# Performance work log

Measured on AMD Instinct MI355X. Metric: run time of the kernel, lower is better.

The kernel has to match this reference:

```python
import jax, jax.numpy as jnp
import numpy as np

NUM_USER = 20000
NUM_ITEM = 20000
N = NUM_USER + NUM_ITEM
E = 250000
DIM_X = 64
NEG_SLOPE = 0.01  # F.leaky_relu default
EPS = 1e-12


def _xavier(key, shape):
    scale = (2.0 / (shape[0] + shape[1])) ** 0.5
    return jax.random.normal(key, shape, dtype=jnp.float32) * scale


def setup_inputs() -> dict:
    key = jax.random.key(0)
    ks = iter(jax.random.split(key, 64))
    inp = {}
    feat_dims = {'v': 2048, 'a': 128, 't': 100}
    lat_dims = {'v': 256, 'a': 128, 't': 100}
    for m in ('v', 'a', 't'):
        Fd, L = feat_dims[m], lat_dims[m]
        inp[m + '_feat'] = jax.random.normal(next(ks), (NUM_ITEM, Fd), dtype=jnp.float32)
        inp[m + '_pref'] = _xavier(next(ks), (NUM_USER, L))
        inp[m + '_mlp_w'] = _xavier(next(ks), (Fd, L))
        inp[m + '_mlp_b'] = jnp.zeros((L,), jnp.float32)
        inp[m + '_conv_w'] = _xavier(next(ks), (L, L))
        inp[m + '_conv_b'] = jnp.zeros((L,), jnp.float32)
        inp[m + '_lin_w'] = _xavier(next(ks), (L, DIM_X))
        inp[m + '_lin_b'] = jnp.zeros((DIM_X,), jnp.float32)
        inp[m + '_g_w'] = _xavier(next(ks), (L, DIM_X))
        inp[m + '_g_b'] = jnp.zeros((DIM_X,), jnp.float32)
    inp['id_emb'] = _xavier(next(ks), (N, DIM_X))
    src = jax.random.randint(next(ks), (E,), 0, NUM_USER)
    dst = jax.random.randint(next(ks), (E,), NUM_USER, N)
    inp['edge_index'] = jnp.stack([src, dst])  # [2, E] user->item
    inp['user_nodes'] = jax.random.randint(next(ks), (1024,), 0, NUM_USER)
    inp['pos_items'] = jax.random.randint(next(ks), (1024,), NUM_USER, N)
    inp['neg_items'] = jax.random.randint(next(ks), (1024,), NUM_USER, N)
    return inp


def _l2norm(x):
    return x / jnp.maximum(jnp.linalg.norm(x, axis=-1, keepdims=True), EPS)


def _graph_gat(x, src, dst, w, b):
    # x: [N, L] -> per-edge gather, gated attention, scatter-add (aggr='add')
    xw = x @ w                      # [N, L]
    x_j = xw[src]                   # source (neighbor) features, [E, L]
    x_i = xw[dst]                   # destination features, [E, L]
    inner = jnp.sum(x_i * x_j, axis=-1)                      # [E]
    deg = jax.ops.segment_sum(jnp.ones_like(inner), src, num_segments=N)
    gate = jax.nn.sigmoid(inner * (deg[src] ** -0.5))        # degree-scaled gate
    logits = inner * gate
    seg_max = jax.ops.segment_max(logits, dst, num_segments=N)
    e = jnp.exp(logits - seg_max[dst])
    denom = jax.ops.segment_sum(e, dst, num_segments=N)
    alpha = e / jnp.maximum(denom[dst], 1e-16)               # softmax over in-edges of dst
    out = jax.ops.segment_sum(x_j * alpha[:, None], dst, num_segments=N)
    return _l2norm(out + b)


def _gnn(feat, pref, mlp_w, mlp_b, conv_w, conv_b, lin_w, lin_b, g_w, g_b, id_emb, src, dst):
    temp = jnp.tanh(feat @ mlp_w + mlp_b)                    # [num_item, L]
    x = _l2norm(jnp.concatenate([pref, temp], axis=0))        # [N, L]
    h = jax.nn.leaky_relu(_graph_gat(x, src, dst, conv_w, conv_b), NEG_SLOPE)
    x_hat = jax.nn.leaky_relu(x @ lin_w + lin_b, NEG_SLOPE) + id_emb
    return jax.nn.leaky_relu(h @ g_w + g_b + x_hat, NEG_SLOPE)  # [N, 64]


def reference(v_feat, a_feat, t_feat,
              v_pref, v_mlp_w, v_mlp_b, v_conv_w, v_conv_b, v_lin_w, v_lin_b, v_g_w, v_g_b,
              a_pref, a_mlp_w, a_mlp_b, a_conv_w, a_conv_b, a_lin_w, a_lin_b, a_g_w, a_g_b,
              t_pref, t_mlp_w, t_mlp_b, t_conv_w, t_conv_b, t_lin_w, t_lin_b, t_g_w, t_g_b,
              id_emb, edge_index, user_nodes, pos_items, neg_items):
    # __init__ doubles the edge list with its reverse (undirected graph)
    ei = jnp.concatenate([edge_index, edge_index[::-1]], axis=1)
    src, dst = ei[0], ei[1]
    v_rep = _gnn(v_feat, v_pref, v_mlp_w, v_mlp_b, v_conv_w, v_conv_b, v_lin_w, v_lin_b, v_g_w, v_g_b, id_emb, src, dst)
    a_rep = _gnn(a_feat, a_pref, a_mlp_w, a_mlp_b, a_conv_w, a_conv_b, a_lin_w, a_lin_b, a_g_w, a_g_b, id_emb, src, dst)
    t_rep = _gnn(t_feat, t_pref, t_mlp_w, t_mlp_b, t_conv_w, t_conv_b, t_lin_w, t_lin_b, t_g_w, t_g_b, id_emb, src, dst)
    rep = (v_rep + a_rep + t_rep) / 3.0                      # [N, 64]
    pos_scores = jnp.sum(rep[user_nodes] * rep[pos_items], axis=1)
    neg_scores = jnp.sum(rep[user_nodes] * rep[neg_items], axis=1)
    return (pos_scores, neg_scores)
```

## Files before the change

kernel.cpp:

```cpp
#include <hip/hip_runtime.h>
#include <math.h>

#define NUSER 20000
#define NITEM 20000
#define NNODE 40000
#define MP_USER 20096
#define MP_NODE 40064

typedef unsigned short u16;
typedef __attribute__((ext_vector_type(8))) short bf16x8;
typedef __attribute__((ext_vector_type(4))) float f32x4;

__device__ __forceinline__ float leaky(float v){ return v > 0.0f ? v : 0.01f*v; }
__device__ __forceinline__ u16 f2bf(float f){
  unsigned u = __float_as_uint(f);
  return (u16)((u + 0x7FFFu + ((u>>16)&1u)) >> 16);
}
__device__ __forceinline__ float bf2f(u16 h){ return __uint_as_float(((unsigned)h)<<16); }
__device__ __forceinline__ unsigned pack2(u16 a, u16 b){ return (unsigned)a | ((unsigned)b<<16); }

enum { EPI_STORE=0, EPI_TANH=1, EPI_LEAKY_ADD=2, EPI_ACCUM=3, EPI_NONE=4 };

template<int WR, int WC, int MI, int EPI, bool ASPLIT, int SPLITK>
__global__ __launch_bounds__(WR*WC*64)
void wgemm_k(const float* __restrict__ A, const u16* __restrict__ Ah, const u16* __restrict__ Al,
             const u16* __restrict__ Bh, const u16* __restrict__ Bl,
             const float* __restrict__ bias, const float* __restrict__ add,
             float* __restrict__ C, int M, int N, int K, int Kp)
{
  constexpr int BM = WR*MI*16, BN = WC*64, T = WR*WC*64, NI = 4;
  __shared__ u16 Ash[4*BM*8], Asl[4*BM*8], Bsh[4*BN*8], Bsl[4*BN*8];
  const int tid = threadIdx.x, lane = tid & 63, wid = tid >> 6;
  const int wrow = wid / WC, wcol = wid % WC;
  const int row0 = blockIdx.y*BM;
  const int fr = lane & 15, kg = lane >> 4;
  const int Kc = Kp / SPLITK;
  const int ks0 = (SPLITK > 1) ? blockIdx.z * Kc : 0;

  f32x4 acc[MI][NI] = {};

  for (int kt = 0; kt < Kc; kt += 32) {
    if (ASPLIT) {
      constexpr int AG = BM*4;
      #pragma unroll
      for (int i = 0; i < 2*AG/T; i++) {
        int g = tid + i*T;
        int gi = (g < AG) ? g : g - AG;
        int r = gi >> 2, kk = gi & 3;
        size_t ofs = (size_t)(row0+r)*Kp + ks0 + kt + kk*8;
        int G = (kk*BM + (r ^ (kk<<1)))*8;
        if (g < AG) *(uint4*)&Ash[G] = *(const uint4*)(Ah + ofs);
        else        *(uint4*)&Asl[G] = *(const uint4*)(Al + ofs);
      }
    } else {
      constexpr int AG = BM*4;
      #pragma unroll
      for (int i = 0; i < AG/T; i++) {
        int g = tid + i*T;
        int r = g >> 2, kk = g & 3;
        int gr = row0 + r, gk = ks0 + kt + kk*8;
        float fv[8];
        if (gr < M && gk + 8 <= K) {
          *(float4*)&fv[0] = *(const float4*)(A + (size_t)gr*K + gk);
          *(float4*)&fv[4] = *(const float4*)(A + (size_t)gr*K + gk + 4);
        } else {
          #pragma unroll
          for (int j=0;j<8;j++) fv[j] = (gr < M && gk + j < K) ? A[(size_t)gr*K + gk + j] : 0.f;
        }
        u16 hs[8], ls[8];
        #pragma unroll
        for (int j=0;j<8;j++){ u16 h = f2bf(fv[j]); hs[j]=h; ls[j]=f2bf(fv[j]-bf2f(h)); }
        int G = (kk*BM + (r ^ (kk<<1)))*8;
        *(uint4*)&Ash[G] = make_uint4(pack2(hs[0],hs[1]),pack2(hs[2],hs[3]),pack2(hs[4],hs[5]),pack2(hs[6],hs[7]));
        *(uint4*)&Asl[G] = make_uint4(pack2(ls[0],ls[1]),pack2(ls[2],ls[3]),pack2(ls[4],ls[5]),pack2(ls[6],ls[7]));
      }
    }
    {
      constexpr int BG = BN*4;
      #pragma unroll
      for (int i = 0; i < 2*BG/T; i++) {
        int g = tid + i*T;
        int gi = (g < BG) ? g : g - BG;
        int r = gi >> 2, kk = gi & 3;
        size_t ofs = (size_t)r*Kp + ks0 + kt + kk*8;
        int G = (kk*BN + (r ^ (kk<<1)))*8;
        if (g < BG) *(uint4*)&Bsh[G] = *(const uint4*)(Bh + ofs);
        else        *(uint4*)&Bsl[G] = *(const uint4*)(Bl + ofs);
      }
    }
    __syncthreads();
    bf16x8 ah_[MI], al_[MI], bh_[NI], bl_[NI];
    #pragma unroll
    for (int mi=0;mi<MI;mi++){
      int rw = wrow*(MI*16) + mi*16 + fr;
      int G = (kg*BM + (rw ^ (kg<<1)))*8;
      ah_[mi] = *(const bf16x8*)&Ash[G];
      al_[mi] = *(const bf16x8*)&Asl[G];
    }
    #pragma unroll
    for (int ni=0;ni<NI;ni++){
      int cw = wcol*64 + ni*16 + fr;
      int G = (kg*BN + (cw ^ (kg<<1)))*8;
      bh_[ni] = *(const bf16x8*)&Bsh[G];
      bl_[ni] = *(const bf16x8*)&Bsl[G];
    }
    #pragma unroll
    for (int mi=0;mi<MI;mi++)
      #pragma unroll
      for (int ni=0;ni<NI;ni++){
        acc[mi][ni] = __builtin_amdgcn_mfma_f32_16x16x32_bf16(ah_[mi], bh_[ni], acc[mi][ni], 0,0,0);
        acc[mi][ni] = __builtin_amdgcn_mfma_f32_16x16x32_bf16(ah_[mi], bl_[ni], acc[mi][ni], 0,0,0);
        acc[mi][ni] = __builtin_amdgcn_mfma_f32_16x16x32_bf16(al_[mi], bh_[ni], acc[mi][ni], 0,0,0);
      }
    __syncthreads();
  }
  float* Cb = (EPI==EPI_NONE) ? (C + (size_t)blockIdx.z*MP_USER*N) : C;
  #pragma unroll
  for (int mi=0;mi<MI;mi++){
    #pragma unroll
    for (int ni=0;ni<NI;ni++){
      int col = wcol*64 + ni*16 + fr;
      if (EPI!=EPI_NONE && col >= N) continue;
      #pragma unroll
      for (int r=0;r<4;r++){
        int row = row0 + wrow*(MI*16) + mi*16 + kg*4 + r;
        if (EPI!=EPI_NONE && row >= M) continue;
        size_t idx = (size_t)row*N + col;
        float v = acc[mi][ni][r];
        if (EPI==EPI_NONE)           Cb[idx] = v;
        else if (EPI==EPI_STORE)     Cb[idx] = v;
        else if (EPI==EPI_TANH)      Cb[idx] = tanhf(v + bias[col]);
        else if (EPI==EPI_LEAKY_ADD) Cb[idx] = leaky(v + bias[col]) + add[idx];
        else                         Cb[idx] += leaky(v + bias[col] + add[idx]);
      }
    }
  }
}

struct WDesc { const float* w; u16 *th, *tl; int K, N, Kp, Np; };
struct WPack { WDesc d[12]; };
__global__ void split_w_k(WPack P)
{
  WDesc D = P.d[blockIdx.y];
  int gid = blockIdx.x*256 + threadIdx.x;
  int tot = D.Np * D.Kp;
  if (gid >= tot) return;
  int k = gid / D.Np, n = gid % D.Np;
  float v = (k < D.K && n < D.N) ? D.w[(size_t)k*D.N + n] : 0.f;
  u16 h = f2bf(v);
  D.th[(size_t)n*D.Kp + k] = h;
  D.tl[(size_t)n*D.Kp + k] = f2bf(v - bf2f(h));
}

__global__ void count_deg(const int* __restrict__ ei, int* __restrict__ deg, int E)
{
  int e = blockIdx.x*blockDim.x + threadIdx.x;
  if (e >= 2*E) return;
  int dst = (e < E) ? ei[e+E] : ei[e-E];
  atomicAdd(&deg[dst], 1);
}

__global__ void scan_rowptr(const int* __restrict__ deg, int* __restrict__ row_ptr, int n)
{
  __shared__ int wsum[4];
  __shared__ int carry;
  int tid = threadIdx.x, lane = tid & 63, wid = tid >> 6;
  if (tid==0) carry = 0;
  __syncthreads();
  for (int base=0; base<n; base+=1024) {
    int i0 = base + tid*4;
    int d[4];
    #pragma unroll
    for (int k=0;k<4;k++) d[k] = (i0+k < n) ? deg[i0+k] : 0;
    int t = d[0]+d[1]+d[2]+d[3];
    int incl = t;
    #pragma unroll
    for (int o=1;o<64;o<<=1){ int v = __shfl_up(incl, o); if (lane >= o) incl += v; }
    if (lane==63) wsum[wid] = incl;
    __syncthreads();
    int pre = carry;
    for (int w=0; w<wid; w++) pre += wsum[w];
    int run = pre + incl - t;
    #pragma unroll
    for (int k=0;k<4;k++){ run += d[k]; if (i0+k < n) row_ptr[i0+k+1] = run; }
    __syncthreads();
    if (tid==0) carry += wsum[0]+wsum[1]+wsum[2]+wsum[3];
  }
  if (tid==0) row_ptr[0] = 0;
}

__global__ void fill_csr(const int* __restrict__ ei, const int* __restrict__ row_ptr,
                         int* __restrict__ row_fill, int* __restrict__ col_src, int E)
{
  int e = blockIdx.x*blockDim.x + threadIdx.x;
  if (e >= 2*E) return;
  int src = ei[e];
  int dst = (e < E) ? ei[e+E] : ei[e-E];
  int pos = row_ptr[dst] + atomicAdd(&row_fill[dst], 1);
  col_src[pos] = src;
}

template<int VW>
__device__ __forceinline__ void loadrow(const float* __restrict__ r, int c0, int L, float* v){
  if (c0 + VW <= L) {
    if (VW==4) *(float4*)v = *(const float4*)r;
    else       *(float2*)v = *(const float2*)r;
  } else {
    #pragma unroll
    for (int j=0;j<VW;j++) v[j] = (c0+j < L) ? r[j] : 0.f;
  }
}

template<int VW>
__global__ __launch_bounds__(256)
void l2norm_split_k(const float* __restrict__ pref, const float* __restrict__ xp,
                    const float* __restrict__ bias,
                    u16* __restrict__ xh, u16* __restrict__ xl, int L, int Kp, int nchunk)
{
  int row = (blockIdx.x*blockDim.x + threadIdx.x) >> 6;
  int lane = threadIdx.x & 63;
  if (row >= MP_NODE) return;
  int c0 = lane*VW;
  size_t ofs = (size_t)row*Kp + c0;
  if (row >= NNODE) {
    if (VW==4) { *(uint2*)&xh[ofs] = make_uint2(0,0); *(uint2*)&xl[ofs] = make_uint2(0,0); }
    else       { *(unsigned*)&xh[ofs] = 0; *(unsigned*)&xl[ofs] = 0; }
    return;
  }
  float v[VW];
  if (row < NUSER) {
    loadrow<VW>(pref + (size_t)row*L + c0, c0, L, v);
  } else {
    int i = row - NUSER;
    size_t po = (size_t)i*Kp + c0;
    float s[VW] = {};
    for (int z = 0; z < nchunk; z++) {
      float a[VW];
      const float* src = xp + (size_t)z*MP_USER*Kp + po;
      if (VW==4) *(float4*)a = *(const float4*)src;
      else       *(float2*)a = *(const float2*)src;
      #pragma unroll
      for (int j=0;j<VW;j++) s[j] += a[j];
    }
    #pragma unroll
    for (int j=0;j<VW;j++){
      int c = c0+j;
      float t = s[j] + ((c<L) ? bias[c] : 0.f);
      v[j] = (c<L) ? tanhf(t) : 0.f;
    }
  }
  float ss = 0.f;
  #pragma unroll
  for (int j=0;j<VW;j++) ss += v[j]*v[j];
  #pragma unroll
  for (int o=32;o;o>>=1) ss += __shfl_xor(ss, o);
  float inv = 1.0f / fmaxf(sqrtf(ss), 1e-12f);
  u16 hs[VW], ls[VW];
  #pragma unroll
  for (int j=0;j<VW;j++){
    float val = (c0+j < L) ? v[j]*inv : 0.f;
    hs[j] = f2bf(val); ls[j] = f2bf(val - bf2f(hs[j]));
  }
  if (VW==4) { *(uint2*)&xh[ofs] = make_uint2(pack2(hs[0],hs[1]),pack2(hs[2],hs[3]));
               *(uint2*)&xl[ofs] = make_uint2(pack2(ls[0],ls[1]),pack2(ls[2],ls[3])); }
  else       { *(unsigned*)&xh[ofs] = pack2(hs[0],hs[1]); *(unsigned*)&xl[ofs] = pack2(ls[0],ls[1]); }
}

template<int VW, int CAP, int LP>
__global__ __launch_bounds__(256)
void fused_edge_k(const float* __restrict__ xw, const int* __restrict__ row_ptr,
                  const int* __restrict__ col_src, const int* __restrict__ deg_,
                  const float* __restrict__ bias, float* __restrict__ glogits,
                  u16* __restrict__ hh, u16* __restrict__ hl, int L, int Kp)
{
  constexpr int KCH = (LP + 63)/64;
  __shared__ float cache[4][CAP][LP];
  __shared__ float lsl[4][64];
  const int slot = threadIdx.x >> 6;
  const int lane = threadIdx.x & 63;
  const int node = blockIdx.x*4 + slot;
  if (node >= MP_NODE) return;
  const int c0 = lane*VW;
  const size_t ofs = (size_t)node*Kp + c0;
  if (node >= NNODE) {
    if (VW==4) { *(uint2*)&hh[ofs] = make_uint2(0,0); *(uint2*)&hl[ofs] = make_uint2(0,0); }
    else       { *(unsigned*)&hh[ofs] = 0; *(unsigned*)&hl[ofs] = 0; }
    return;
  }
  const int s = row_ptr[node], e = row_ptr[node+1];
  const int cnt = e - s;
  const int sw = lane >> 4, j = lane & 15;
  const bool big = (cnt > 64);

  const float* pd = xw + (size_t)node*L;
  float4 pdv[KCH];
  #pragma unroll
  for (int k=0;k<KCH;k++){
    int c = j*4 + k*64;
    pdv[k] = (c < L) ? *(const float4*)(pd + c) : make_float4(0.f,0.f,0.f,0.f);
  }

  int nit = (cnt + 3) >> 2;
  for (int it = 0; it < nit; it++) {
    int i = it*4 + sw;
    float dot = 0.f;
    int src = 0;
    if (i < cnt) {
      src = col_src[s+i];
      const float* ps = xw + (size_t)src*L;
      #pragma unroll
      for (int k=0;k<KCH;k++){
        int c = j*4 + k*64;
        if (c < L) {
          float4 a = *(const float4*)(ps + c);
          if (i < CAP) *(float4*)&cache[slot][i][c] = a;
          dot += a.x*pdv[k].x + a.y*pdv[k].y + a.z*pdv[k].z + a.w*pdv[k].w;
        }
      }
    }
    #pragma unroll
    for (int o=8;o;o>>=1) dot += __shfl_xor(dot, o, 16);
    if (i < cnt && j == 0) {
      float t = dot / sqrtf((float)deg_[src]);
      float gate = 1.0f/(1.0f + expf(-t));
      float lg = dot * gate;
      if (i < 64) lsl[slot][i] = lg;
      if (big) glogits[s+i] = lg;
    }
  }
  asm volatile("s_waitcnt lgkmcnt(0)" ::: "memory");

  float alpha_r = 0.f, mxv = 0.f, sinv = 0.f;
  if (!big) {
    if (cnt > 0) {
      float lv = (lane < cnt) ? lsl[slot][lane] : -INFINITY;
      float m = lv;
      #pragma unroll
      for (int o=32;o;o>>=1) m = fmaxf(m, __shfl_xor(m, o));
      float el = (lane < cnt) ? expf(lv - m) : 0.f;
      float d = el;
      #pragma unroll
      for (int o=32;o;o>>=1) d += __shfl_xor(d, o);
      alpha_r = el / fmaxf(d, 1e-16f);
    }
  } else {
    asm volatile("s_waitcnt vmcnt(0)" ::: "memory");
    float m = -INFINITY;
    for (int q=s+lane;q<e;q+=64) m = fmaxf(m, glogits[q]);
    #pragma unroll
    for (int o=32;o;o>>=1) m = fmaxf(m, __shfl_xor(m, o));
    float d = 0.f;
    for (int q=s+lane;q<e;q+=64) d += expf(glogits[q]-m);
    #pragma unroll
    for (int o=32;o;o>>=1) d += __shfl_xor(d, o);
    mxv = m; sinv = 1.0f/fmaxf(d, 1e-16f);
  }

  float acc[VW] = {};
  for (int i = 0; i < cnt; i++) {
    float a = big ? (expf(glogits[s+i]-mxv)*sinv) : __shfl(alpha_r, i);
    float v[VW];
    if (i < CAP) {
      if (c0 + VW <= L) {
        if (VW==4) *(float4*)v = *(const float4*)&cache[slot][i][c0];
        else       *(float2*)v = *(const float2*)&cache[slot][i][c0];
      } else {
        #pragma unroll
        for (int jj=0;jj<VW;jj++) v[jj] = (c0+jj < L) ? cache[slot][i][c0+jj] : 0.f;
      }
    } else {
      loadrow<VW>(xw + (size_t)col_src[s+i]*L + c0, c0, L, v);
    }
    #pragma unroll
    for (int jj=0;jj<VW;jj++) acc[jj] = fmaf(a, v[jj], acc[jj]);
  }
  float t[VW], ss = 0.f;
  #pragma unroll
  for (int jj=0;jj<VW;jj++){ int c = c0+jj; t[jj] = (c<L) ? acc[jj]+bias[c] : 0.f; ss += t[jj]*t[jj]; }
  #pragma unroll
  for (int o=32;o;o>>=1) ss += __shfl_xor(ss, o);
  float inv = 1.0f / fmaxf(sqrtf(ss), 1e-12f);
  u16 hs[VW], ls[VW];
  #pragma unroll
  for (int jj=0;jj<VW;jj++){
    float o2 = (c0+jj < L) ? leaky(t[jj]*inv) : 0.f;
    hs[jj] = f2bf(o2); ls[jj] = f2bf(o2 - bf2f(hs[jj]));
  }
  if (VW==4) { *(uint2*)&hh[ofs] = make_uint2(pack2(hs[0],hs[1]),pack2(hs[2],hs[3]));
               *(uint2*)&hl[ofs] = make_uint2(pack2(ls[0],ls[1]),pack2(ls[2],ls[3])); }
  else       { *(unsigned*)&hh[ofs] = pack2(hs[0],hs[1]); *(unsigned*)&hl[ofs] = pack2(ls[0],ls[1]); }
}

__global__ __launch_bounds__(256)
void score_k(const float* __restrict__ rep, const int* __restrict__ un,
             const int* __restrict__ pi, const int* __restrict__ ni, float* __restrict__ out)
{
  int wid = (blockIdx.x*blockDim.x + threadIdx.x) >> 6;
  int lane = threadIdx.x & 63;
  if (wid >= 2048) return;
  int i = wid & 1023;
  int isneg = wid >> 10;
  int u = un[i];
  int it = isneg ? ni[i] : pi[i];
  float p = rep[(size_t)u*64 + lane] * rep[(size_t)it*64 + lane];
  #pragma unroll
  for (int o=32;o;o>>=1) p += __shfl_xor(p, o);
  if (lane==0) out[isneg*1024 + i] = p * (1.0f/9.0f);
}

static inline size_t align_up(size_t v){ return (v + 255) & ~(size_t)255; }
static inline int cdiv(int a, int b){ return (a + b - 1) / b; }

extern "C" void kernel_launch(void* const* d_in, const int* in_sizes, int n_in,
                              void* d_out, int out_size, void* d_ws, size_t ws_size,
                              hipStream_t stream)
{
  const int E  = in_sizes[31] / 2;
  const int E2 = 2*E;

  char* p = (char*)d_ws;
  auto carve = [&](size_t bytes){ char* r = p; p += align_up(bytes); return r; };
  float* xw     = (float*)carve((size_t)4*MP_USER*256*4);
  float* xp     = xw;
  u16*   xh     = (u16*)carve((size_t)MP_NODE*256*2);
  u16*   xl     = (u16*)carve((size_t)MP_NODE*256*2);
  float* xhat   = (float*)carve((size_t)NNODE*64*4);
  float* rep    = (float*)carve((size_t)NNODE*64*4);
  float* logits = (float*)carve((size_t)E2*4);
  int* deg      = (int*)carve((size_t)NNODE*4);
  int* row_ptr  = (int*)carve((size_t)(NNODE+1)*4);
  int* row_fill = (int*)carve((size_t)NNODE*4);
  int* col_src  = (int*)carve((size_t)E2*4);

  const int* ei = (const int*)d_in[31];
  const float* id_emb = (const float*)d_in[30];

  struct Mod { const float *feat,*pref,*mlp_w,*mlp_b,*conv_w,*conv_b,*lin_w,*lin_b,*g_w,*g_b;
               int Fd, L, Kpx, Kpf, NpL; };
  Mod md[3];
  for (int m=0;m<3;m++) {
    int b = m*10;
    md[m].feat   = (const float*)d_in[b+0];
    md[m].pref   = (const float*)d_in[b+1];
    md[m].mlp_w  = (const float*)d_in[b+2];
    md[m].mlp_b  = (const float*)d_in[b+3];
    md[m].conv_w = (const float*)d_in[b+4];
    md[m].conv_b = (const float*)d_in[b+5];
    md[m].lin_w  = (const float*)d_in[b+6];
    md[m].lin_b  = (const float*)d_in[b+7];
    md[m].g_w    = (const float*)d_in[b+8];
    md[m].g_b    = (const float*)d_in[b+9];
  }
  md[0].Fd=2048; md[0].L=256; md[0].Kpx=256; md[0].Kpf=2048; md[0].NpL=256;
  md[1].Fd=128;  md[1].L=128; md[1].Kpx=128; md[1].Kpf=128;  md[1].NpL=128;
  md[2].Fd=100;  md[2].L=100; md[2].Kpx=128; md[2].Kpf=128;  md[2].NpL=128;

  u16 *wmh[3],*wml[3],*wch[3],*wcl[3],*wlh[3],*wll[3],*wgh[3],*wgl[3];
  WPack P;
  int maxTot = 0;
  for (int m=0;m<3;m++) {
    const Mod& M_ = md[m];
    size_t smlp = (size_t)M_.NpL*M_.Kpf*2, sconv = (size_t)M_.NpL*M_.Kpx*2, slin = (size_t)64*M_.Kpx*2;
    wmh[m]=(u16*)carve(smlp); wml[m]=(u16*)carve(smlp);
    wch[m]=(u16*)carve(sconv); wcl[m]=(u16*)carve(sconv);
    wlh[m]=(u16*)carve(slin);  wll[m]=(u16*)carve(slin);
    wgh[m]=(u16*)carve(slin);  wgl[m]=(u16*)carve(slin);
    P.d[m*4+0] = { M_.mlp_w,  wmh[m], wml[m], M_.Fd, M_.L, M_.Kpf, M_.NpL };
    P.d[m*4+1] = { M_.conv_w, wch[m], wcl[m], M_.L,  M_.L, M_.Kpx, M_.NpL };
    P.d[m*4+2] = { M_.lin_w,  wlh[m], wll[m], M_.L,  64,   M_.Kpx, 64 };
    P.d[m*4+3] = { M_.g_w,    wgh[m], wgl[m], M_.L,  64,   M_.Kpx, 64 };
    for (int q=0;q<4;q++){ int t = P.d[m*4+q].Np*P.d[m*4+q].Kp; if (t>maxTot) maxTot=t; }
  }

  hipMemsetAsync(deg, 0, (size_t)NNODE*4, stream);
  hipMemsetAsync(row_fill, 0, (size_t)NNODE*4, stream);
  hipMemsetAsync(rep, 0, (size_t)NNODE*64*4, stream);

  { dim3 g(cdiv(maxTot,256), 12); split_w_k<<<g,256,0,stream>>>(P); }
  {
    int blocks = cdiv(E2, 256);
    count_deg<<<blocks,256,0,stream>>>(ei, deg, E);
    scan_rowptr<<<1,256,0,stream>>>(deg, row_ptr, NNODE);
    fill_csr<<<blocks,256,0,stream>>>(ei, row_ptr, row_fill, col_src, E);
  }

  for (int m=0;m<3;m++) {
    const Mod& M_ = md[m];
    const int L = M_.L;

    if (m == 0)
      wgemm_k<1,4,4,EPI_NONE,false,4><<<dim3(1,MP_USER/64,4),256,0,stream>>>(
          M_.feat, nullptr, nullptr, wmh[m], wml[m], nullptr, nullptr,
          xp, NUSER, 256, M_.Fd, M_.Kpf);
    else
      wgemm_k<1,2,4,EPI_NONE,false,2><<<dim3(1,MP_USER/64,2),128,0,stream>>>(
          M_.feat, nullptr, nullptr, wmh[m], wml[m], nullptr, nullptr,
          xp, NUSER, 128, M_.Fd, M_.Kpf);

    {
      int nchunk = (m==0) ? 4 : 2;
      if (M_.Kpx==256) l2norm_split_k<4><<<MP_NODE/4,256,0,stream>>>(M_.pref, xp, M_.mlp_b, xh, xl, L, M_.Kpx, nchunk);
      else             l2norm_split_k<2><<<MP_NODE/4,256,0,stream>>>(M_.pref, xp, M_.mlp_b, xh, xl, L, M_.Kpx, nchunk);
    }

    if (m == 0)
      wgemm_k<1,4,4,EPI_STORE,true,1><<<dim3(1,MP_NODE/64,1),256,0,stream>>>(
          nullptr, xh, xl, wch[m], wcl[m], nullptr, nullptr, xw, NNODE, L, L, M_.Kpx);
    else
      wgemm_k<1,2,4,EPI_STORE,true,1><<<dim3(1,MP_NODE/64,1),128,0,stream>>>(
          nullptr, xh, xl, wch[m], wcl[m], nullptr, nullptr, xw, NNODE, L, L, M_.Kpx);

    wgemm_k<4,1,2,EPI_LEAKY_ADD,true,1><<<dim3(1,MP_NODE/128,1),256,0,stream>>>(
        nullptr, xh, xl, wlh[m], wll[m], M_.lin_b, id_emb, xhat, NNODE, 64, L, M_.Kpx);

    if (m == 0)
      fused_edge_k<4,12,256><<<MP_NODE/4,256,0,stream>>>(xw, row_ptr, col_src, deg, M_.conv_b, logits, xh, xl, L, M_.Kpx);
    else if (m == 1)
      fused_edge_k<2,20,128><<<MP_NODE/4,256,0,stream>>>(xw, row_ptr, col_src, deg, M_.conv_b, logits, xh, xl, L, M_.Kpx);
    else
      fused_edge_k<2,20,104><<<MP_NODE/4,256,0,stream>>>(xw, row_ptr, col_src, deg, M_.conv_b, logits, xh, xl, L, M_.Kpx);

    wgemm_k<4,1,2,EPI_ACCUM,true,1><<<dim3(1,MP_NODE/128,1),256,0,stream>>>(
        nullptr, xh, xl, wgh[m], wgl[m], M_.g_b, xhat, rep, NNODE, 64, L, M_.Kpx);
  }

  score_k<<<cdiv(2048*64,256),256,0,stream>>>(rep, (const int*)d_in[32], (const int*)d_in[33],
                                              (const int*)d_in[34], (float*)d_out);
}
```

Measured before the change: 1.243 ms.

## Replace two-pass edge softmax with single-pass online softmax aggregation

The per-node edge kernel now computes gated logits and accumulates the weighted neighbor rows in a single pass using an online (running max) softmax. Each 16-lane subgroup keeps its own accumulator, and the subgroups are merged with cross-lane shuffles. This removes the shared-memory row cache, the global logits buffer used for high-degree nodes, and the second pass over neighbors. In exchange it adds per-edge exp rescaling of the register accumulators and more registers per thread, which may lower occupancy.

```diff
diff --git a/kernel.cpp b/kernel.cpp
--- a/kernel.cpp
+++ b/kernel.cpp
@@ -266,31 +266,31 @@
   else       { *(unsigned*)&xh[ofs] = pack2(hs[0],hs[1]); *(unsigned*)&xl[ofs] = pack2(ls[0],ls[1]); }
 }
 
-template<int VW, int CAP, int LP>
+template<int KCH>
 __global__ __launch_bounds__(256)
 void fused_edge_k(const float* __restrict__ xw, const int* __restrict__ row_ptr,
                   const int* __restrict__ col_src, const int* __restrict__ deg_,
-                  const float* __restrict__ bias, float* __restrict__ glogits,
+                  const float* __restrict__ bias,
                   u16* __restrict__ hh, u16* __restrict__ hl, int L, int Kp)
 {
-  constexpr int KCH = (LP + 63)/64;
-  __shared__ float cache[4][CAP][LP];
-  __shared__ float lsl[4][64];
-  const int slot = threadIdx.x >> 6;
   const int lane = threadIdx.x & 63;
-  const int node = blockIdx.x*4 + slot;
+  const int node = blockIdx.x*4 + (threadIdx.x >> 6);
   if (node >= MP_NODE) return;
-  const int c0 = lane*VW;
-  const size_t ofs = (size_t)node*Kp + c0;
+  const int sw = lane >> 4, j = lane & 15;
+
   if (node >= NNODE) {
-    if (VW==4) { *(uint2*)&hh[ofs] = make_uint2(0,0); *(uint2*)&hl[ofs] = make_uint2(0,0); }
-    else       { *(unsigned*)&hh[ofs] = 0; *(unsigned*)&hl[ofs] = 0; }
+    if (sw == 0) {
+      #pragma unroll
+      for (int k=0;k<KCH;k++){
+        int c = j*4 + k*64;
+        *(uint2*)&hh[(size_t)node*Kp + c] = make_uint2(0,0);
+        *(uint2*)&hl[(size_t)node*Kp + c] = make_uint2(0,0);
+      }
+    }
     return;
   }
   const int s = row_ptr[node], e = row_ptr[node+1];
   const int cnt = e - s;
-  const int sw = lane >> 4, j = lane & 15;
-  const bool big = (cnt > 64);
 
   const float* pd = xw + (size_t)node*L;
   float4 pdv[KCH];
@@ -300,95 +300,112 @@
     pdv[k] = (c < L) ? *(const float4*)(pd + c) : make_float4(0.f,0.f,0.f,0.f);
   }
 
-  int nit = (cnt + 3) >> 2;
+  float m = -1e30f, d = 0.f;
+  float4 acc[KCH];
+  #pragma unroll
+  for (int k=0;k<KCH;k++) acc[k] = make_float4(0.f,0.f,0.f,0.f);
+
+  const int nit = (cnt + 3) >> 2;
   for (int it = 0; it < nit; it++) {
     int i = it*4 + sw;
+    bool valid = (i < cnt);
+    float4 row[KCH];
+    #pragma unroll
+    for (int k=0;k<KCH;k++) row[k] = make_float4(0.f,0.f,0.f,0.f);
     float dot = 0.f;
     int src = 0;
-    if (i < cnt) {
+    if (valid) {
       src = col_src[s+i];
       const float* ps = xw + (size_t)src*L;
       #pragma unroll
       for (int k=0;k<KCH;k++){
         int c = j*4 + k*64;
         if (c < L) {
-          float4 a = *(const float4*)(ps + c);
-          if (i < CAP) *(float4*)&cache[slot][i][c] = a;
-          dot += a.x*pdv[k].x + a.y*pdv[k].y + a.z*pdv[k].z + a.w*pdv[k].w;
+          row[k] = *(const float4*)(ps + c);
+          dot += row[k].x*pdv[k].x + row[k].y*pdv[k].y + row[k].z*pdv[k].z + row[k].w*pdv[k].w;
         }
       }
     }
     #pragma unroll
     for (int o=8;o;o>>=1) dot += __shfl_xor(dot, o, 16);
-    if (i < cnt && j == 0) {
+    float lg = -1e30f;
+    if (valid) {
       float t = dot / sqrtf((float)deg_[src]);
       float gate = 1.0f/(1.0f + expf(-t));
-      float lg = dot * gate;
-      if (i < 64) lsl[slot][i] = lg;
-      if (big) glogits[s+i] = lg;
-    }
-  }
-  asm volatile("s_waitcnt lgkmcnt(0)" ::: "memory");
-
-  float alpha_r = 0.f, mxv = 0.f, sinv = 0.f;
-  if (!big) {
-    if (cnt > 0) {
-      float lv = (lane < cnt) ? lsl[slot][lane] : -INFINITY;
-      float m = lv;
-      #pragma unroll
-      for (int o=32;o;o>>=1) m = fmaxf(m, __shfl_xor(m, o));
-      float el = (lane < cnt) ? expf(lv - m) : 0.f;
-      float d = el;
-      #pragma unroll
-      for (int o=32;o;o>>=1) d += __shfl_xor(d, o);
-      alpha_r = el / fmaxf(d, 1e-16f);
-    }
-  } else {
-    asm volatile("s_waitcnt vmcnt(0)" ::: "memory");
-    float m = -INFINITY;
-    for (int q=s+lane;q<e;q+=64) m = fmaxf(m, glogits[q]);
-    #pragma unroll
-    for (int o=32;o;o>>=1) m = fmaxf(m, __shfl_xor(m, o));
-    float d = 0.f;
-    for (int q=s+lane;q<e;q+=64) d += expf(glogits[q]-m);
-    #pragma unroll
-    for (int o=32;o;o>>=1) d += __shfl_xor(d, o);
-    mxv = m; sinv = 1.0f/fmaxf(d, 1e-16f);
-  }
-
-  float acc[VW] = {};
-  for (int i = 0; i < cnt; i++) {
-    float a = big ? (expf(glogits[s+i]-mxv)*sinv) : __shfl(alpha_r, i);
-    float v[VW];
-    if (i < CAP) {
-      if (c0 + VW <= L) {
-        if (VW==4) *(float4*)v = *(const float4*)&cache[slot][i][c0];
-        else       *(float2*)v = *(const float2*)&cache[slot][i][c0];
-      } else {
-        #pragma unroll
-        for (int jj=0;jj<VW;jj++) v[jj] = (c0+jj < L) ? cache[slot][i][c0+jj] : 0.f;
-      }
+      lg = dot * gate;
+    }
+    float mn = fmaxf(m, lg);
+    float sc = expf(m - mn);
+    float w  = expf(lg - mn);
+    d = d*sc + w;
+    #pragma unroll
+    for (int k=0;k<KCH;k++){
+      acc[k].x = acc[k].x*sc + w*row[k].x;
+      acc[k].y = acc[k].y*sc + w*row[k].y;
+      acc[k].z = acc[k].z*sc + w*row[k].z;
+      acc[k].w = acc[k].w*sc + w*row[k].w;
+    }
+    m = mn;
+  }
+
+  #pragma unroll
+  for (int off=16; off<=32; off<<=1) {
+    float m2 = __shfl_xor(m, off);
+    float d2 = __shfl_xor(d, off);
+    float4 a2[KCH];
+    #pragma unroll
+    for (int k=0;k<KCH;k++){
+      a2[k].x = __shfl_xor(acc[k].x, off);
+      a2[k].y = __shfl_xor(acc[k].y, off);
+      a2[k].z = __shfl_xor(acc[k].z, off);
+      a2[k].w = __shfl_xor(acc[k].w, off);
+    }
+    float mn = fmaxf(m, m2);
+    float s1 = expf(m - mn), s2 = expf(m2 - mn);
+    d = d*s1 + d2*s2;
+    #pragma unroll
+    for (int k=0;k<KCH;k++){
+      acc[k].x = acc[k].x*s1 + a2[k].x*s2;
+      acc[k].y = acc[k].y*s1 + a2[k].y*s2;
+      acc[k].z = acc[k].z*s1 + a2[k].z*s2;
+      acc[k].w = acc[k].w*s1 + a2[k].w*s2;
+    }
+    m = mn;
+  }
+
+  float dinv = 1.0f / fmaxf(d, 1e-16f);
+
+  float ss = 0.f;
+  float4 tv[KCH];
+  #pragma unroll
+  for (int k=0;k<KCH;k++){
+    int c = j*4 + k*64;
+    if (c < L) {
+      float4 bv = *(const float4*)(bias + c);
+      tv[k].x = acc[k].x*dinv + bv.x;
+      tv[k].y = acc[k].y*dinv + bv.y;
+      tv[k].z = acc[k].z*dinv + bv.z;
+      tv[k].w = acc[k].w*dinv + bv.w;
     } else {
-      loadrow<VW>(xw + (size_t)col_src[s+i]*L + c0, c0, L, v);
-    }
-    #pragma unroll
-    for (int jj=0;jj<VW;jj++) acc[jj] = fmaf(a, v[jj], acc[jj]);
-  }
-  float t[VW], ss = 0.f;
-  #pragma unroll
-  for (int jj=0;jj<VW;jj++){ int c = c0+jj; t[jj] = (c<L) ? acc[jj]+bias[c] : 0.f; ss += t[jj]*t[jj]; }
-  #pragma unroll
-  for (int o=32;o;o>>=1) ss += __shfl_xor(ss, o);
+      tv[k] = make_float4(0.f,0.f,0.f,0.f);
+    }
+    ss += tv[k].x*tv[k].x + tv[k].y*tv[k].y + tv[k].z*tv[k].z + tv[k].w*tv[k].w;
+  }
+  #pragma unroll
+  for (int o=1;o<16;o<<=1) ss += __shfl_xor(ss, o, 16);
   float inv = 1.0f / fmaxf(sqrtf(ss), 1e-12f);
-  u16 hs[VW], ls[VW];
-  #pragma unroll
-  for (int jj=0;jj<VW;jj++){
-    float o2 = (c0+jj < L) ? leaky(t[jj]*inv) : 0.f;
-    hs[jj] = f2bf(o2); ls[jj] = f2bf(o2 - bf2f(hs[jj]));
-  }
-  if (VW==4) { *(uint2*)&hh[ofs] = make_uint2(pack2(hs[0],hs[1]),pack2(hs[2],hs[3]));
-               *(uint2*)&hl[ofs] = make_uint2(pack2(ls[0],ls[1]),pack2(ls[2],ls[3])); }
-  else       { *(unsigned*)&hh[ofs] = pack2(hs[0],hs[1]); *(unsigned*)&hl[ofs] = pack2(ls[0],ls[1]); }
+  if (sw == 0) {
+    #pragma unroll
+    for (int k=0;k<KCH;k++){
+      int c = j*4 + k*64;
+      float o0 = leaky(tv[k].x*inv), o1 = leaky(tv[k].y*inv);
+      float o2 = leaky(tv[k].z*inv), o3 = leaky(tv[k].w*inv);
+      u16 h0=f2bf(o0), h1=f2bf(o1), h2=f2bf(o2), h3=f2bf(o3);
+      u16 l0=f2bf(o0-bf2f(h0)), l1=f2bf(o1-bf2f(h1)), l2=f2bf(o2-bf2f(h2)), l3=f2bf(o3-bf2f(h3));
+      *(uint2*)&hh[(size_t)node*Kp + c] = make_uint2(pack2(h0,h1), pack2(h2,h3));
+      *(uint2*)&hl[(size_t)node*Kp + c] = make_uint2(pack2(l0,l1), pack2(l2,l3));
+    }
+  }
 }
 
 __global__ __launch_bounds__(256)
@@ -426,7 +443,6 @@
   u16*   xl     = (u16*)carve((size_t)MP_NODE*256*2);
   float* xhat   = (float*)carve((size_t)NNODE*64*4);
   float* rep    = (float*)carve((size_t)NNODE*64*4);
-  float* logits = (float*)carve((size_t)E2*4);
   int* deg      = (int*)carve((size_t)NNODE*4);
   int* row_ptr  = (int*)carve((size_t)(NNODE+1)*4);
   int* row_fill = (int*)carve((size_t)NNODE*4);
@@ -514,11 +530,9 @@
         nullptr, xh, xl, wlh[m], wll[m], M_.lin_b, id_emb, xhat, NNODE, 64, L, M_.Kpx);
 
     if (m == 0)
-      fused_edge_k<4,12,256><<<MP_NODE/4,256,0,stream>>>(xw, row_ptr, col_src, deg, M_.conv_b, logits, xh, xl, L, M_.Kpx);
-    else if (m == 1)
-      fused_edge_k<2,20,128><<<MP_NODE/4,256,0,stream>>>(xw, row_ptr, col_src, deg, M_.conv_b, logits, xh, xl, L, M_.Kpx);
+      fused_edge_k<4><<<MP_NODE/4,256,0,stream>>>(xw, row_ptr, col_src, deg, M_.conv_b, xh, xl, L, M_.Kpx);
     else
-      fused_edge_k<2,20,104><<<MP_NODE/4,256,0,stream>>>(xw, row_ptr, col_src, deg, M_.conv_b, logits, xh, xl, L, M_.Kpx);
+      fused_edge_k<2><<<MP_NODE/4,256,0,stream>>>(xw, row_ptr, col_src, deg, M_.conv_b, xh, xl, L, M_.Kpx);
 
     wgemm_k<4,1,2,EPI_ACCUM,true,1><<<dim3(1,MP_NODE/128,1),256,0,stream>>>(
         nullptr, xh, xl, wgh[m], wgl[m], M_.g_b, xhat, rep, NNODE, 64, L, M_.Kpx);
```

Measured after the change: 1.009 ms. 18.8% less time.
